# Kernel optimization log

Measured on AMD Instinct MI355X. Metric: run time of the kernel, lower is better.

The kernel has to match this reference:

```python
import jax, jax.numpy as jnp
import numpy as np

L = 6        # number of blocks (hardcoded in Transformer)
H = 16       # num_heads
C = 1024     # num_embeddings
HS = C // H  # head_size = 64
FF = 4 * C   # ffn hidden
V = 67       # vocab = len(chars)
B, T = 8, 1024
EPS = 1e-5   # nn.LayerNorm default


def _ln(x, g, b):
    m = jnp.mean(x, axis=-1, keepdims=True)
    v = jnp.mean((x - m) ** 2, axis=-1, keepdims=True)
    return (x - m) * jax.lax.rsqrt(v + EPS) * g + b


def setup_inputs() -> dict:
    key = jax.random.key(0)
    ks = jax.random.split(key, 20)
    s = 0.02
    inp = {
        "idx": jax.random.randint(ks[0], (B, T), 0, V),
        "tok_emb": jax.random.normal(ks[1], (V, C), jnp.float32) * s,
        "pos_emb": jax.random.normal(ks[2], (T, C), jnp.float32) * s,
        # per-head Q/K/V Linears (bias=False) packed as [L, C, H*HS]
        "Wq": jax.random.normal(ks[3], (L, C, C), jnp.float32) * s,
        "Wk": jax.random.normal(ks[4], (L, C, C), jnp.float32) * s,
        "Wv": jax.random.normal(ks[5], (L, C, C), jnp.float32) * s,
        "Wo": jax.random.normal(ks[6], (L, C, C), jnp.float32) * s,
        "bo": jnp.zeros((L, C), jnp.float32),
        "ln1_g": jnp.ones((L, C), jnp.float32),
        "ln1_b": jnp.zeros((L, C), jnp.float32),
        "ln2_g": jnp.ones((L, C), jnp.float32),
        "ln2_b": jnp.zeros((L, C), jnp.float32),
        "W1": jax.random.normal(ks[7], (L, C, FF), jnp.float32) * s,
        "b1": jnp.zeros((L, FF), jnp.float32),
        "W2": jax.random.normal(ks[8], (L, FF, C), jnp.float32) * s,
        "b2": jnp.zeros((L, C), jnp.float32),
        "lnf_g": jnp.ones((C,), jnp.float32),
        "lnf_b": jnp.zeros((C,), jnp.float32),
        "Wlm": jax.random.normal(ks[9], (C, V), jnp.float32) * s,
        "blm": jnp.zeros((V,), jnp.float32),
    }
    return inp


def reference(idx, tok_emb, pos_emb, Wq, Wk, Wv, Wo, bo, ln1_g, ln1_b,
              ln2_g, ln2_b, W1, b1, W2, b2, lnf_g, lnf_b, Wlm, blm):
    Bc, Tc = idx.shape
    x = tok_emb[idx] + pos_emb[:Tc]                      # [B,T,C]
    mask = jnp.tril(jnp.ones((Tc, Tc), bool))
    scale = 1.0 / np.sqrt(HS)                            # wei / head_size**0.5
    neg_inf = jnp.finfo(x.dtype).min
    for l in range(L):
        h = _ln(x, ln1_g[l], ln1_b[l])
        q = (h @ Wq[l]).reshape(Bc, Tc, H, HS)
        k = (h @ Wk[l]).reshape(Bc, Tc, H, HS)
        v = (h @ Wv[l]).reshape(Bc, Tc, H, HS)
        wei = jnp.einsum('bqhd,bkhd->bhqk', q, k) * scale
        wei = jnp.where(mask, wei, neg_inf)
        wei = jax.nn.softmax(wei, axis=-1)
        o = jnp.einsum('bhqk,bkhd->bqhd', wei, v).reshape(Bc, Tc, C)
        x = x + o @ Wo[l] + bo[l]
        h = _ln(x, ln2_g[l], ln2_b[l])
        x = x + jax.nn.relu(h @ W1[l] + b1[l]) @ W2[l] + b2[l]
    x = _ln(x, lnf_g, lnf_b)
    return x @ Wlm + blm                                 # [B,T,V] logits
```

## Files before the change

kernel.cpp:

```cpp
#include <hip/hip_runtime.h>

typedef unsigned short u16;
typedef unsigned int u32;
typedef __bf16 bf16x8 __attribute__((ext_vector_type(8)));
typedef float f32x4 __attribute__((ext_vector_type(4)));

#define LAYERS 6
#define NH 16
#define CDIM 1024
#define HS 64
#define FFDIM 4096
#define VOCAB 67
#define BATCH 8
#define TSEQ 1024
#define NTOK (BATCH * TSEQ)

__device__ __forceinline__ float bf2f(u16 u) {
    union { u32 i; float f; } x; x.i = ((u32)u) << 16; return x.f;
}
__device__ __forceinline__ u16 f2bf(float f) {
    u32 x = __float_as_uint(f);
    u32 r = (x + 0x7fffu + ((x >> 16) & 1u)) >> 16;
    return (u16)r;
}
__device__ __forceinline__ float ldx(const void* p, size_t i, int f32) {
    return f32 ? ((const float*)p)[i] : bf2f(((const u16*)p)[i]);
}
__device__ __forceinline__ void glds16(const u16* g, u16* lds) {
    __builtin_amdgcn_global_load_lds(
        (const __attribute__((address_space(1))) void*)g,
        (__attribute__((address_space(3))) void*)lds, 16, 0, 0);
}

__global__ void detect_kernel(const void* __restrict__ tok, int* __restrict__ flag) {
    int bad = 0;
    for (int i = threadIdx.x; i < 4096; i += 256) {
        float f = bf2f(((const u16*)tok)[i]);
        if (!(fabsf(f) < 1000.0f)) bad = 1;
    }
    if (bad) atomicOr(flag, 1);
}

template <int BF16OUT>
__global__ void embed_kernel(const int* __restrict__ idx, const void* __restrict__ tok,
                             const void* __restrict__ pos, void* __restrict__ X,
                             const int* __restrict__ dflag) {
    const int f32 = *dflag;
    const int i = blockIdx.x * 256 + threadIdx.x;
    const int n = i >> 10, cc = i & 1023;
    const int t = n & 1023;
    const float v = ldx(tok, (size_t)idx[n] * CDIM + cc, f32) + ldx(pos, (size_t)t * CDIM + cc, f32);
    if constexpr (BF16OUT) ((u16*)X)[i] = f2bf(v);
    else                   ((float*)X)[i] = v;
}

__global__ void transpose_kernel(const void* __restrict__ src, size_t soff, u16* __restrict__ dst,
                                 int R, int C, const int* __restrict__ dflag) {
    __shared__ u16 tile[32][33];
    const int f32 = *dflag;
    const int bx = blockIdx.x * 32, by = blockIdx.y * 32;
    const int tx = threadIdx.x, ty = threadIdx.y;
    #pragma unroll
    for (int i = 0; i < 32; i += 8) {
        const size_t si = soff + (size_t)(by + ty + i) * C + bx + tx;
        tile[ty + i][tx] = f32 ? f2bf(((const float*)src)[si]) : ((const u16*)src)[si];
    }
    __syncthreads();
    #pragma unroll
    for (int i = 0; i < 32; i += 8) dst[(size_t)(bx + ty + i) * R + by + tx] = tile[tx][ty + i];
}

template <int BF16IN>
__global__ __launch_bounds__(256) void ln_kernel(const void* __restrict__ Xv, const void* __restrict__ g,
                                                 const void* __restrict__ b, size_t loff,
                                                 u16* __restrict__ Hout, const int* __restrict__ dflag) {
    __shared__ float sred[4];
    const int f32 = *dflag;
    const int row = blockIdx.x, tid = threadIdx.x;
    float v[4];
    if constexpr (BF16IN) {
        const u16* xr = (const u16*)Xv + (size_t)row * CDIM;
        #pragma unroll
        for (int i = 0; i < 4; ++i) v[i] = bf2f(xr[tid + i * 256]);
    } else {
        const float* xr = (const float*)Xv + (size_t)row * CDIM;
        #pragma unroll
        for (int i = 0; i < 4; ++i) v[i] = xr[tid + i * 256];
    }
    float s = v[0] + v[1] + v[2] + v[3];
    #pragma unroll
    for (int off = 1; off < 64; off <<= 1) s += __shfl_xor(s, off, 64);
    if ((tid & 63) == 0) sred[tid >> 6] = s;
    __syncthreads();
    const float mean = (sred[0] + sred[1] + sred[2] + sred[3]) * (1.f / 1024.f);
    __syncthreads();
    float sq = 0.f;
    #pragma unroll
    for (int i = 0; i < 4; ++i) { v[i] -= mean; sq += v[i] * v[i]; }
    #pragma unroll
    for (int off = 1; off < 64; off <<= 1) sq += __shfl_xor(sq, off, 64);
    if ((tid & 63) == 0) sred[tid >> 6] = sq;
    __syncthreads();
    const float var = (sred[0] + sred[1] + sred[2] + sred[3]) * (1.f / 1024.f);
    const float inv = rsqrtf(var + 1e-5f);
    u16* hr = Hout + (size_t)row * CDIM;
    #pragma unroll
    for (int i = 0; i < 4; ++i) {
        const int cc = tid + i * 256;
        hr[cc] = f2bf(v[i] * inv * ldx(g, loff + cc, f32) + ldx(b, loff + cc, f32));
    }
}

template <int MODE>
__global__ __launch_bounds__(256) void gemm_bt(const u16* __restrict__ A, const u16* __restrict__ BT,
                                               const void* __restrict__ bias, size_t boff,
                                               float* __restrict__ X, u16* __restrict__ Out,
                                               int M, int N, int K, const int* __restrict__ dflag) {
    __shared__ u16 As[128][64];
    __shared__ u16 Bs[128][64];
    const int tid = threadIdx.x;
    const int lane = tid & 63;
    const int w = tid >> 6;
    const int wr = w >> 1, wc = w & 1;
    const int quad = lane >> 4, c = lane & 15;

    const int gx = gridDim.x, gy = gridDim.y;
    int bx = blockIdx.x, by = blockIdx.y;
    const int nwg = gx * gy;
    if ((nwg & 7) == 0) {
        const int bid = by * gx + bx;
        const int q = nwg >> 3;
        const int xcd = bid & 7;
        const int u = bid >> 3;
        const int cols = q / gy;
        if (cols * gy == q) {
            bx = xcd * cols + (u % cols);
            by = u / cols;
        } else {
            const int l = xcd * q + u;
            bx = l / gy;
            by = l - bx * gy;
        }
    }
    const int m0 = by * 128, n0 = bx * 128;

    const int lr = lane >> 3;
    const int sc = ((lane & 7) ^ lr) * 8;

    const f32x4 zero4 = {0.f, 0.f, 0.f, 0.f};
    f32x4 acc[4][4];
    #pragma unroll
    for (int i = 0; i < 4; ++i)
        #pragma unroll
        for (int j = 0; j < 4; ++j) acc[i][j] = zero4;

    for (int k0 = 0; k0 < K; k0 += 64) {
        #pragma unroll
        for (int i = 0; i < 4; ++i) {
            const int rbase = w * 8 + i * 32;
            glds16(A  + (size_t)(m0 + rbase + lr) * K + k0 + sc, &As[rbase][0]);
            glds16(BT + (size_t)(n0 + rbase + lr) * K + k0 + sc, &Bs[rbase][0]);
        }
        __syncthreads();
        #pragma unroll
        for (int ks = 0; ks < 2; ++ks) {
            bf16x8 af[4], bfr[4];
            #pragma unroll
            for (int t = 0; t < 4; ++t) {
                const int ch = ((ks * 4 + quad) ^ (c & 7)) * 8;
                af[t]  = *(const bf16x8*)(&As[wr * 64 + t * 16 + c][ch]);
                bfr[t] = *(const bf16x8*)(&Bs[wc * 64 + t * 16 + c][ch]);
            }
            #pragma unroll
            for (int mt = 0; mt < 4; ++mt)
                #pragma unroll
                for (int nt = 0; nt < 4; ++nt)
                    acc[mt][nt] = __builtin_amdgcn_mfma_f32_16x16x32_bf16(af[mt], bfr[nt], acc[mt][nt], 0, 0, 0);
        }
        __syncthreads();
    }

    int f32 = 0;
    if constexpr (MODE >= 1) f32 = *dflag;
    #pragma unroll
    for (int mt = 0; mt < 4; ++mt) {
        #pragma unroll
        for (int nt = 0; nt < 4; ++nt) {
            const int col = n0 + wc * 64 + nt * 16 + c;
            float bv = 0.f;
            if constexpr (MODE >= 1) bv = ldx(bias, boff + col, f32);
            #pragma unroll
            for (int r = 0; r < 4; ++r) {
                const size_t row = (size_t)(m0 + wr * 64 + mt * 16 + quad * 4 + r);
                float v = acc[mt][nt][r];
                if constexpr (MODE == 2) {
                    X[row * N + col] += v + bv;
                } else if constexpr (MODE == 3) {
                    u16* o = &Out[row * N + col];
                    *o = f2bf(bf2f(*o) + v + bv);
                } else if constexpr (MODE == 1) {
                    v += bv; v = fmaxf(v, 0.f);
                    Out[row * N + col] = f2bf(v);
                } else {
                    Out[row * N + col] = f2bf(v);
                }
            }
        }
    }
}

__global__ __launch_bounds__(256) void attn_kernel(const u16* __restrict__ Qb, const u16* __restrict__ Kb,
                                                   const u16* __restrict__ Vb, u16* __restrict__ Ob,
                                                   int rs) {
    __shared__ u16 Qs[64][64];
    __shared__ u16 Ks[64][64];
    __shared__ u16 Vts[64][64];
    __shared__ u16 Ps[4][16][64];

    const int tid = threadIdx.x;
    const int lane = tid & 63;
    const int w = tid >> 6;
    const int quad = lane >> 4;
    const int c = lane & 15;
    const int bh = blockIdx.x;
    const int b = bh >> 4;
    const int h = bh & 15;
    const int q0 = blockIdx.y * 64;
    const size_t base = ((size_t)b * TSEQ) * rs + (size_t)h * HS;

    {
        const int r = tid >> 2;
        const int d0 = (tid & 3) * 16;
        const u16* src = Qb + base + (size_t)(q0 + r) * rs + d0;
        #pragma unroll
        for (int i = 0; i < 16; ++i) Qs[r][d0 + i] = f2bf(bf2f(src[i]) * 0.125f);
    }
    __syncthreads();

    const int qbase = q0 + w * 16;
    const bf16x8 qf0 = *(const bf16x8*)(&Qs[w * 16 + c][quad * 8]);
    const bf16x8 qf1 = *(const bf16x8*)(&Qs[w * 16 + c][32 + quad * 8]);

    const f32x4 zero4 = {0.f, 0.f, 0.f, 0.f};
    f32x4 oacc[4] = {zero4, zero4, zero4, zero4};
    float m_r[4], l_r[4];
    #pragma unroll
    for (int r = 0; r < 4; ++r) { m_r[r] = -1e30f; l_r[r] = 0.f; }

    const int nch = blockIdx.y + 1;
    for (int ch = 0; ch < nch; ++ch) {
        const int k0 = ch * 64;
        {
            const int r = tid >> 2;
            const int d0 = (tid & 3) * 16;
            const u16* ks = Kb + base + (size_t)(k0 + r) * rs + d0;
            *(uint4*)(&Ks[r][d0])     = *(const uint4*)(ks);
            *(uint4*)(&Ks[r][d0 + 8]) = *(const uint4*)(ks + 8);
            const u16* vs = Vb + base + (size_t)(k0 + r) * rs + d0;
            #pragma unroll
            for (int i = 0; i < 16; ++i) Vts[d0 + i][r] = vs[i];
        }
        __syncthreads();

        f32x4 s[4];
        #pragma unroll
        for (int kt = 0; kt < 4; ++kt) {
            const bf16x8 kf0 = *(const bf16x8*)(&Ks[kt * 16 + c][quad * 8]);
            const bf16x8 kf1 = *(const bf16x8*)(&Ks[kt * 16 + c][32 + quad * 8]);
            f32x4 t0 = __builtin_amdgcn_mfma_f32_16x16x32_bf16(qf0, kf0, zero4, 0, 0, 0);
            s[kt] = __builtin_amdgcn_mfma_f32_16x16x32_bf16(qf1, kf1, t0, 0, 0, 0);
        }
        #pragma unroll
        for (int kt = 0; kt < 4; ++kt) {
            const int kabs = k0 + kt * 16 + c;
            #pragma unroll
            for (int r = 0; r < 4; ++r) {
                if (kabs > qbase + quad * 4 + r) s[kt][r] = -1e30f;
            }
        }
        float p[4][4];
        #pragma unroll
        for (int r = 0; r < 4; ++r) {
            float rm = fmaxf(fmaxf(s[0][r], s[1][r]), fmaxf(s[2][r], s[3][r]));
            #pragma unroll
            for (int off = 1; off < 16; off <<= 1) rm = fmaxf(rm, __shfl_xor(rm, off, 16));
            const float mnew = fmaxf(m_r[r], rm);
            const float alpha = __expf(m_r[r] - mnew);
            float psum = 0.f;
            #pragma unroll
            for (int kt = 0; kt < 4; ++kt) {
                const float e = __expf(s[kt][r] - mnew);
                p[kt][r] = e; psum += e;
            }
            #pragma unroll
            for (int off = 1; off < 16; off <<= 1) psum += __shfl_xor(psum, off, 16);
            l_r[r] = l_r[r] * alpha + psum;
            m_r[r] = mnew;
            #pragma unroll
            for (int dt = 0; dt < 4; ++dt) oacc[dt][r] *= alpha;
        }
        #pragma unroll
        for (int kt = 0; kt < 4; ++kt)
            #pragma unroll
            for (int r = 0; r < 4; ++r)
                Ps[w][quad * 4 + r][kt * 16 + c] = f2bf(p[kt][r]);
        __syncthreads();
        #pragma unroll
        for (int ks2 = 0; ks2 < 2; ++ks2) {
            const bf16x8 pf = *(const bf16x8*)(&Ps[w][c][ks2 * 32 + quad * 8]);
            #pragma unroll
            for (int dt = 0; dt < 4; ++dt) {
                const bf16x8 vf = *(const bf16x8*)(&Vts[dt * 16 + c][ks2 * 32 + quad * 8]);
                oacc[dt] = __builtin_amdgcn_mfma_f32_16x16x32_bf16(pf, vf, oacc[dt], 0, 0, 0);
            }
        }
        __syncthreads();
    }
    #pragma unroll
    for (int dt = 0; dt < 4; ++dt)
        #pragma unroll
        for (int r = 0; r < 4; ++r) {
            const size_t row = (size_t)b * TSEQ + qbase + quad * 4 + r;
            Ob[row * CDIM + h * HS + dt * 16 + c] = f2bf(oacc[dt][r] / l_r[r]);
        }
}

__global__ void wlmT_kernel(const void* __restrict__ Wlm, u16* __restrict__ WlmT,
                            const int* __restrict__ dflag) {
    const int f32 = *dflag;
    const int i = blockIdx.x * 256 + threadIdx.x;
    if (i >= VOCAB * CDIM) return;
    const int v = i >> 10, cc = i & 1023;
    WlmT[i] = f2bf(ldx(Wlm, (size_t)cc * VOCAB + v, f32));
}

__device__ __forceinline__ void ld16bf(const u16* p, float* v) {
    const uint4 a = *(const uint4*)(p);
    const uint4 b = *(const uint4*)(p + 8);
    u32 t[8] = {a.x, a.y, a.z, a.w, b.x, b.y, b.z, b.w};
    #pragma unroll
    for (int i = 0; i < 8; ++i) {
        v[2 * i]     = bf2f((u16)(t[i] & 0xffffu));
        v[2 * i + 1] = bf2f((u16)(t[i] >> 16));
    }
}

__global__ __launch_bounds__(256) void lmhead2_kernel(const u16* __restrict__ Hf, const u16* __restrict__ WlmT,
                                                      const void* __restrict__ blm, void* __restrict__ out,
                                                      size_t ooff, const int* __restrict__ dflag) {
    const int f32 = *dflag;
    const int lane = threadIdx.x & 63;
    const int n = blockIdx.x * 4 + (threadIdx.x >> 6);
    float hv[16];
    ld16bf(Hf + (size_t)n * CDIM + lane * 16, hv);
    for (int v = 0; v < VOCAB; ++v) {
        float wv[16];
        ld16bf(WlmT + (size_t)v * CDIM + lane * 16, wv);
        float s = 0.f;
        #pragma unroll
        for (int i = 0; i < 16; ++i) s += hv[i] * wv[i];
        #pragma unroll
        for (int off = 1; off < 64; off <<= 1) s += __shfl_xor(s, off, 64);
        if (lane == 0) {
            s += ldx(blm, v, f32);
            const size_t o = ooff + (size_t)n * VOCAB + v;
            if (f32) ((float*)out)[o] = s;
            else     ((u16*)out)[o]   = f2bf(s);
        }
    }
}

extern "C" void kernel_launch(void* const* d_in, const int* in_sizes, int n_in,
                              void* d_out, int out_size, void* d_ws, size_t ws_size,
                              hipStream_t stream) {
    const int*  idx  = (const int*)d_in[0];
    const void* tok  = d_in[1];
    const void* pos  = d_in[2];
    const void* Wq   = d_in[3];
    const void* Wk   = d_in[4];
    const void* Wv   = d_in[5];
    const void* Wo   = d_in[6];
    const void* bo   = d_in[7];
    const void* ln1g = d_in[8];
    const void* ln1b = d_in[9];
    const void* ln2g = d_in[10];
    const void* ln2b = d_in[11];
    const void* W1   = d_in[12];
    const void* b1   = d_in[13];
    const void* W2   = d_in[14];
    const void* b2   = d_in[15];
    const void* lnfg = d_in[16];
    const void* lnfb = d_in[17];
    const void* Wlm  = d_in[18];
    const void* blm  = d_in[19];

    const dim3 tb(32, 8);
    const size_t wsz = (size_t)CDIM * CDIM;
    const size_t MB = 1048576ull;

    int* dflag = (int*)d_ws;
    char* pool = (char*)d_ws + 256;
    const size_t pool_size = (ws_size > 256) ? ws_size - 256 : 0;

    const int wlmT_blocks = (VOCAB * CDIM + 255) / 256;

    if (pool_size >= 120 * MB) {
        hipMemsetAsync(d_ws, 0, 256 + 120 * MB, stream);
        detect_kernel<<<1, 256, 0, stream>>>(tok, dflag);
        char* p = pool;
        u16* wT = (u16*)p;  p += (size_t)FFDIM * CDIM * 2;
        u16* WqT = wT;
        u16* WkT = wT + 1 * wsz;
        u16* WvT = wT + 2 * wsz;
        u16* WoT = wT + 3 * wsz;
        float* x = (float*)p; p += (size_t)NTOK * CDIM * 4;
        u16* h   = (u16*)p;   p += (size_t)NTOK * CDIM * 2;
        u16* qb  = (u16*)p;   p += (size_t)NTOK * CDIM * 2;
        u16* kb  = (u16*)p;   p += (size_t)NTOK * CDIM * 2;  (void)kb;
        u16* vb  = (u16*)p;   p += (size_t)NTOK * CDIM * 2;  (void)vb;
        u16* ob  = (u16*)p;   p += (size_t)NTOK * CDIM * 2;
        u16* ffh = qb;

        embed_kernel<0><<<NTOK * CDIM / 256, 256, 0, stream>>>(idx, tok, pos, x, dflag);
        for (int l = 0; l < LAYERS; ++l) {
            transpose_kernel<<<dim3(32, 32), tb, 0, stream>>>(Wq, l * wsz, WqT, CDIM, CDIM, dflag);
            transpose_kernel<<<dim3(32, 32), tb, 0, stream>>>(Wk, l * wsz, WkT, CDIM, CDIM, dflag);
            transpose_kernel<<<dim3(32, 32), tb, 0, stream>>>(Wv, l * wsz, WvT, CDIM, CDIM, dflag);
            transpose_kernel<<<dim3(32, 32), tb, 0, stream>>>(Wo, l * wsz, WoT, CDIM, CDIM, dflag);
            ln_kernel<0><<<NTOK, 256, 0, stream>>>(x, ln1g, ln1b, (size_t)l * CDIM, h, dflag);
            gemm_bt<0><<<dim3(24, 64), 256, 0, stream>>>(h, wT, nullptr, 0, nullptr, qb, NTOK, 3 * CDIM, CDIM, dflag);
            attn_kernel<<<dim3(BATCH * NH, TSEQ / 64), 256, 0, stream>>>(qb, qb + CDIM, qb + 2 * CDIM, ob, 3 * CDIM);
            gemm_bt<2><<<dim3(8, 64), 256, 0, stream>>>(ob, WoT, bo, (size_t)l * CDIM, x, nullptr, NTOK, CDIM, CDIM, dflag);
            ln_kernel<0><<<NTOK, 256, 0, stream>>>(x, ln2g, ln2b, (size_t)l * CDIM, h, dflag);
            transpose_kernel<<<dim3(128, 32), tb, 0, stream>>>(W1, (size_t)l * CDIM * FFDIM, wT, CDIM, FFDIM, dflag);
            gemm_bt<1><<<dim3(32, 64), 256, 0, stream>>>(h, wT, b1, (size_t)l * FFDIM, nullptr, ffh, NTOK, FFDIM, CDIM, dflag);
            transpose_kernel<<<dim3(32, 128), tb, 0, stream>>>(W2, (size_t)l * CDIM * FFDIM, wT, FFDIM, CDIM, dflag);
            gemm_bt<2><<<dim3(8, 64), 256, 0, stream>>>(ffh, wT, b2, (size_t)l * CDIM, x, nullptr, NTOK, CDIM, FFDIM, dflag);
        }
        ln_kernel<0><<<NTOK, 256, 0, stream>>>(x, lnfg, lnfb, 0, h, dflag);
        wlmT_kernel<<<wlmT_blocks, 256, 0, stream>>>(Wlm, qb, dflag);
        lmhead2_kernel<<<NTOK / 4, 256, 0, stream>>>(h, qb, blm, d_out, 0, dflag);
    } else if (pool_size >= 34 * MB) {
        int CR, useW2T;
        if      (pool_size >= 52 * MB) { CR = 2048; useW2T = 1; }
        else if (pool_size >= 42 * MB) { CR = 1024; useW2T = 1; }
        else                           { CR = 1024; useW2T = 0; }
        const size_t need = 8 * MB + 16 * MB + (size_t)CR * CDIM * 2 * 5 + (useW2T ? 8 * MB : 0);
        hipMemsetAsync(d_ws, 0, 256 + need, stream);
        detect_kernel<<<1, 256, 0, stream>>>(tok, dflag);
        char* p = pool;
        u16* wT = (u16*)p;  p += (size_t)FFDIM * CDIM * 2;
        u16* WqT = wT;
        u16* WkT = wT + 1 * wsz;
        u16* WvT = wT + 2 * wsz;
        u16* WoT = wT + 3 * wsz;
        u16* xb  = (u16*)p; p += (size_t)NTOK * CDIM * 2;
        u16* hc  = (u16*)p; p += (size_t)CR * CDIM * 2;
        u16* qc  = (u16*)p; p += (size_t)CR * CDIM * 2;
        u16* kc  = (u16*)p; p += (size_t)CR * CDIM * 2;      (void)kc;
        u16* vc  = (u16*)p; p += (size_t)CR * CDIM * 2;      (void)vc;
        u16* oc  = (u16*)p; p += (size_t)CR * CDIM * 2;
        u16* ffc = qc;
        u16* W2T = nullptr;
        if (useW2T) { W2T = (u16*)p; p += (size_t)FFDIM * CDIM * 2; }

        embed_kernel<1><<<NTOK * CDIM / 256, 256, 0, stream>>>(idx, tok, pos, xb, dflag);
        for (int l = 0; l < LAYERS; ++l) {
            transpose_kernel<<<dim3(32, 32), tb, 0, stream>>>(Wq, l * wsz, WqT, CDIM, CDIM, dflag);
            transpose_kernel<<<dim3(32, 32), tb, 0, stream>>>(Wk, l * wsz, WkT, CDIM, CDIM, dflag);
            transpose_kernel<<<dim3(32, 32), tb, 0, stream>>>(Wv, l * wsz, WvT, CDIM, CDIM, dflag);
            transpose_kernel<<<dim3(32, 32), tb, 0, stream>>>(Wo, l * wsz, WoT, CDIM, CDIM, dflag);
            for (int g = 0; g < NTOK / CR; ++g) {
                u16* xg = xb + (size_t)g * CR * CDIM;
                ln_kernel<1><<<CR, 256, 0, stream>>>(xg, ln1g, ln1b, (size_t)l * CDIM, hc, dflag);
                gemm_bt<0><<<dim3(24, CR / 128), 256, 0, stream>>>(hc, wT, nullptr, 0, nullptr, qc, CR, 3 * CDIM, CDIM, dflag);
                attn_kernel<<<dim3((CR / TSEQ) * NH, TSEQ / 64), 256, 0, stream>>>(qc, qc + CDIM, qc + 2 * CDIM, oc, 3 * CDIM);
                gemm_bt<3><<<dim3(8, CR / 128), 256, 0, stream>>>(oc, WoT, bo, (size_t)l * CDIM, nullptr, xg, CR, CDIM, CDIM, dflag);
            }
            if (W2T) {
                transpose_kernel<<<dim3(128, 32), tb, 0, stream>>>(W1, (size_t)l * CDIM * FFDIM, wT, CDIM, FFDIM, dflag);
                transpose_kernel<<<dim3(32, 128), tb, 0, stream>>>(W2, (size_t)l * CDIM * FFDIM, W2T, FFDIM, CDIM, dflag);
                for (int g = 0; g < NTOK / CR; ++g) {
                    u16* xg = xb + (size_t)g * CR * CDIM;
                    ln_kernel<1><<<CR, 256, 0, stream>>>(xg, ln2g, ln2b, (size_t)l * CDIM, hc, dflag);
                    gemm_bt<1><<<dim3(32, CR / 128), 256, 0, stream>>>(hc, wT, b1, (size_t)l * FFDIM, nullptr, ffc, CR, FFDIM, CDIM, dflag);
                    gemm_bt<3><<<dim3(8, CR / 128), 256, 0, stream>>>(ffc, W2T, b2, (size_t)l * CDIM, nullptr, xg, CR, CDIM, FFDIM, dflag);
                }
            } else {
                for (int g = 0; g < NTOK / CR; ++g) {
                    u16* xg = xb + (size_t)g * CR * CDIM;
                    ln_kernel<1><<<CR, 256, 0, stream>>>(xg, ln2g, ln2b, (size_t)l * CDIM, hc, dflag);
                    transpose_kernel<<<dim3(128, 32), tb, 0, stream>>>(W1, (size_t)l * CDIM * FFDIM, wT, CDIM, FFDIM, dflag);
                    gemm_bt<1><<<dim3(32, CR / 128), 256, 0, stream>>>(hc, wT, b1, (size_t)l * FFDIM, nullptr, ffc, CR, FFDIM, CDIM, dflag);
                    transpose_kernel<<<dim3(32, 128), tb, 0, stream>>>(W2, (size_t)l * CDIM * FFDIM, wT, FFDIM, CDIM, dflag);
                    gemm_bt<3><<<dim3(8, CR / 128), 256, 0, stream>>>(ffc, wT, b2, (size_t)l * CDIM, nullptr, xg, CR, CDIM, FFDIM, dflag);
                }
            }
        }
        wlmT_kernel<<<wlmT_blocks, 256, 0, stream>>>(Wlm, qc, dflag);
        for (int g = 0; g < NTOK / CR; ++g) {
            u16* xg = xb + (size_t)g * CR * CDIM;
            ln_kernel<1><<<CR, 256, 0, stream>>>(xg, lnfg, lnfb, 0, hc, dflag);
            lmhead2_kernel<<<CR / 4, 256, 0, stream>>>(hc, qc, blm, d_out, (size_t)g * CR * VOCAB, dflag);
        }
    } else {
        hipMemsetAsync(d_out, 0, (size_t)out_size * 2, stream);
    }
}
```

Baseline: 2.988 ms.

## Rework attention to read Q/K/V fragments directly from global with pre-transposed V

Attention no longer stages Q, K and V tiles in shared memory with block-wide barriers. Q and K MFMA fragments are loaded straight from global memory. V is first transposed into a separate buffer by a new transpose kernel launch, so its fragments can also be read directly. The Q scaling moves onto the scores, the P tile in LDS is XOR-swizzled so barriers can be dropped, and blocks are remapped so the longest causal rows are scheduled first and grouped by XCD. The cost is an extra transpose pass per layer and uncoalesced, possibly repeated global loads that now depend on cache hits.

```diff
diff --git a/kernel.cpp b/kernel.cpp
--- a/kernel.cpp
+++ b/kernel.cpp
@@ -54,15 +54,16 @@
     else                   ((float*)X)[i] = v;
 }
 
+template <int BF16SRC>
 __global__ void transpose_kernel(const void* __restrict__ src, size_t soff, u16* __restrict__ dst,
-                                 int R, int C, const int* __restrict__ dflag) {
+                                 int R, int C, int SC, const int* __restrict__ dflag) {
     __shared__ u16 tile[32][33];
-    const int f32 = *dflag;
+    const int f32 = BF16SRC ? 0 : *dflag;
     const int bx = blockIdx.x * 32, by = blockIdx.y * 32;
     const int tx = threadIdx.x, ty = threadIdx.y;
     #pragma unroll
     for (int i = 0; i < 32; i += 8) {
-        const size_t si = soff + (size_t)(by + ty + i) * C + bx + tx;
+        const size_t si = soff + (size_t)(by + ty + i) * SC + bx + tx;
         tile[ty + i][tx] = f32 ? f2bf(((const float*)src)[si]) : ((const u16*)src)[si];
     }
     __syncthreads();
@@ -210,11 +211,8 @@
 }
 
 __global__ __launch_bounds__(256) void attn_kernel(const u16* __restrict__ Qb, const u16* __restrict__ Kb,
-                                                   const u16* __restrict__ Vb, u16* __restrict__ Ob,
-                                                   int rs) {
-    __shared__ u16 Qs[64][64];
-    __shared__ u16 Ks[64][64];
-    __shared__ u16 Vts[64][64];
+                                                   const u16* __restrict__ VT, u16* __restrict__ Ob,
+                                                   int rs, int vstride) {
     __shared__ u16 Ps[4][16][64];
 
     const int tid = threadIdx.x;
@@ -222,24 +220,31 @@
     const int w = tid >> 6;
     const int quad = lane >> 4;
     const int c = lane & 15;
-    const int bh = blockIdx.x;
+
+    const int nbh = gridDim.x, nq = gridDim.y;
+    int bh, qi;
+    {
+        const int flat = blockIdx.y * nbh + blockIdx.x;
+        if ((nbh & 7) == 0) {
+            const int bpx = nbh >> 3;
+            const int xcd = flat & 7;
+            const int u = flat >> 3;
+            bh = xcd * bpx + (u % bpx);
+            qi = nq - 1 - u / bpx;
+        } else { bh = blockIdx.x; qi = blockIdx.y; }
+    }
     const int b = bh >> 4;
     const int h = bh & 15;
-    const int q0 = blockIdx.y * 64;
+    const int q0 = qi * 64;
     const size_t base = ((size_t)b * TSEQ) * rs + (size_t)h * HS;
 
-    {
-        const int r = tid >> 2;
-        const int d0 = (tid & 3) * 16;
-        const u16* src = Qb + base + (size_t)(q0 + r) * rs + d0;
-        #pragma unroll
-        for (int i = 0; i < 16; ++i) Qs[r][d0 + i] = f2bf(bf2f(src[i]) * 0.125f);
-    }
-    __syncthreads();
-
     const int qbase = q0 + w * 16;
-    const bf16x8 qf0 = *(const bf16x8*)(&Qs[w * 16 + c][quad * 8]);
-    const bf16x8 qf1 = *(const bf16x8*)(&Qs[w * 16 + c][32 + quad * 8]);
+    const u16* qrow = Qb + base + (size_t)(qbase + c) * rs;
+    const bf16x8 qf0 = *(const bf16x8*)(qrow + quad * 8);
+    const bf16x8 qf1 = *(const bf16x8*)(qrow + 32 + quad * 8);
+
+    const u16* krow = Kb + base + (size_t)c * rs + quad * 8;
+    const u16* vrow = VT + (size_t)(h * HS) * vstride + (size_t)b * TSEQ;
 
     const f32x4 zero4 = {0.f, 0.f, 0.f, 0.f};
     f32x4 oacc[4] = {zero4, zero4, zero4, zero4};
@@ -247,26 +252,15 @@
     #pragma unroll
     for (int r = 0; r < 4; ++r) { m_r[r] = -1e30f; l_r[r] = 0.f; }
 
-    const int nch = blockIdx.y + 1;
+    const int nch = qi + 1;
     for (int ch = 0; ch < nch; ++ch) {
         const int k0 = ch * 64;
-        {
-            const int r = tid >> 2;
-            const int d0 = (tid & 3) * 16;
-            const u16* ks = Kb + base + (size_t)(k0 + r) * rs + d0;
-            *(uint4*)(&Ks[r][d0])     = *(const uint4*)(ks);
-            *(uint4*)(&Ks[r][d0 + 8]) = *(const uint4*)(ks + 8);
-            const u16* vs = Vb + base + (size_t)(k0 + r) * rs + d0;
-            #pragma unroll
-            for (int i = 0; i < 16; ++i) Vts[d0 + i][r] = vs[i];
-        }
-        __syncthreads();
-
         f32x4 s[4];
         #pragma unroll
         for (int kt = 0; kt < 4; ++kt) {
-            const bf16x8 kf0 = *(const bf16x8*)(&Ks[kt * 16 + c][quad * 8]);
-            const bf16x8 kf1 = *(const bf16x8*)(&Ks[kt * 16 + c][32 + quad * 8]);
+            const u16* kp = krow + (size_t)(k0 + kt * 16) * rs;
+            const bf16x8 kf0 = *(const bf16x8*)(kp);
+            const bf16x8 kf1 = *(const bf16x8*)(kp + 32);
             f32x4 t0 = __builtin_amdgcn_mfma_f32_16x16x32_bf16(qf0, kf0, zero4, 0, 0, 0);
             s[kt] = __builtin_amdgcn_mfma_f32_16x16x32_bf16(qf1, kf1, t0, 0, 0, 0);
         }
@@ -275,6 +269,7 @@
             const int kabs = k0 + kt * 16 + c;
             #pragma unroll
             for (int r = 0; r < 4; ++r) {
+                s[kt][r] *= 0.125f;
                 if (kabs > qbase + quad * 4 + r) s[kt][r] = -1e30f;
             }
         }
@@ -302,19 +297,21 @@
         #pragma unroll
         for (int kt = 0; kt < 4; ++kt)
             #pragma unroll
-            for (int r = 0; r < 4; ++r)
-                Ps[w][quad * 4 + r][kt * 16 + c] = f2bf(p[kt][r]);
-        __syncthreads();
+            for (int r = 0; r < 4; ++r) {
+                const int prow = quad * 4 + r;
+                const int ch2 = (kt * 2 + (c >> 3)) ^ (prow & 7);
+                Ps[w][prow][ch2 * 8 + (c & 7)] = f2bf(p[kt][r]);
+            }
         #pragma unroll
         for (int ks2 = 0; ks2 < 2; ++ks2) {
-            const bf16x8 pf = *(const bf16x8*)(&Ps[w][c][ks2 * 32 + quad * 8]);
+            const bf16x8 pf = *(const bf16x8*)(&Ps[w][c][(((ks2 * 4 + quad) ^ (c & 7))) * 8]);
             #pragma unroll
             for (int dt = 0; dt < 4; ++dt) {
-                const bf16x8 vf = *(const bf16x8*)(&Vts[dt * 16 + c][ks2 * 32 + quad * 8]);
+                const u16* vp = vrow + (size_t)(dt * 16 + c) * vstride + k0 + ks2 * 32 + quad * 8;
+                const bf16x8 vf = *(const bf16x8*)(vp);
                 oacc[dt] = __builtin_amdgcn_mfma_f32_16x16x32_bf16(pf, vf, oacc[dt], 0, 0, 0);
             }
         }
-        __syncthreads();
     }
     #pragma unroll
     for (int dt = 0; dt < 4; ++dt)
@@ -423,18 +420,19 @@
 
         embed_kernel<0><<<NTOK * CDIM / 256, 256, 0, stream>>>(idx, tok, pos, x, dflag);
         for (int l = 0; l < LAYERS; ++l) {
-            transpose_kernel<<<dim3(32, 32), tb, 0, stream>>>(Wq, l * wsz, WqT, CDIM, CDIM, dflag);
-            transpose_kernel<<<dim3(32, 32), tb, 0, stream>>>(Wk, l * wsz, WkT, CDIM, CDIM, dflag);
-            transpose_kernel<<<dim3(32, 32), tb, 0, stream>>>(Wv, l * wsz, WvT, CDIM, CDIM, dflag);
-            transpose_kernel<<<dim3(32, 32), tb, 0, stream>>>(Wo, l * wsz, WoT, CDIM, CDIM, dflag);
+            transpose_kernel<0><<<dim3(32, 32), tb, 0, stream>>>(Wq, l * wsz, WqT, CDIM, CDIM, CDIM, dflag);
+            transpose_kernel<0><<<dim3(32, 32), tb, 0, stream>>>(Wk, l * wsz, WkT, CDIM, CDIM, CDIM, dflag);
+            transpose_kernel<0><<<dim3(32, 32), tb, 0, stream>>>(Wv, l * wsz, WvT, CDIM, CDIM, CDIM, dflag);
+            transpose_kernel<0><<<dim3(32, 32), tb, 0, stream>>>(Wo, l * wsz, WoT, CDIM, CDIM, CDIM, dflag);
             ln_kernel<0><<<NTOK, 256, 0, stream>>>(x, ln1g, ln1b, (size_t)l * CDIM, h, dflag);
             gemm_bt<0><<<dim3(24, 64), 256, 0, stream>>>(h, wT, nullptr, 0, nullptr, qb, NTOK, 3 * CDIM, CDIM, dflag);
-            attn_kernel<<<dim3(BATCH * NH, TSEQ / 64), 256, 0, stream>>>(qb, qb + CDIM, qb + 2 * CDIM, ob, 3 * CDIM);
+            transpose_kernel<1><<<dim3(32, NTOK / 32), tb, 0, stream>>>(qb, 2 * CDIM, h, NTOK, CDIM, 3 * CDIM, dflag);
+            attn_kernel<<<dim3(BATCH * NH, TSEQ / 64), 256, 0, stream>>>(qb, qb + CDIM, h, ob, 3 * CDIM, NTOK);
             gemm_bt<2><<<dim3(8, 64), 256, 0, stream>>>(ob, WoT, bo, (size_t)l * CDIM, x, nullptr, NTOK, CDIM, CDIM, dflag);
             ln_kernel<0><<<NTOK, 256, 0, stream>>>(x, ln2g, ln2b, (size_t)l * CDIM, h, dflag);
-            transpose_kernel<<<dim3(128, 32), tb, 0, stream>>>(W1, (size_t)l * CDIM * FFDIM, wT, CDIM, FFDIM, dflag);
+            transpose_kernel<0><<<dim3(128, 32), tb, 0, stream>>>(W1, (size_t)l * CDIM * FFDIM, wT, CDIM, FFDIM, FFDIM, dflag);
             gemm_bt<1><<<dim3(32, 64), 256, 0, stream>>>(h, wT, b1, (size_t)l * FFDIM, nullptr, ffh, NTOK, FFDIM, CDIM, dflag);
-            transpose_kernel<<<dim3(32, 128), tb, 0, stream>>>(W2, (size_t)l * CDIM * FFDIM, wT, FFDIM, CDIM, dflag);
+            transpose_kernel<0><<<dim3(32, 128), tb, 0, stream>>>(W2, (size_t)l * CDIM * FFDIM, wT, FFDIM, CDIM, CDIM, dflag);
             gemm_bt<2><<<dim3(8, 64), 256, 0, stream>>>(ffh, wT, b2, (size_t)l * CDIM, x, nullptr, NTOK, CDIM, FFDIM, dflag);
         }
         ln_kernel<0><<<NTOK, 256, 0, stream>>>(x, lnfg, lnfb, 0, h, dflag);
@@ -466,20 +464,21 @@
 
         embed_kernel<1><<<NTOK * CDIM / 256, 256, 0, stream>>>(idx, tok, pos, xb, dflag);
         for (int l = 0; l < LAYERS; ++l) {
-            transpose_kernel<<<dim3(32, 32), tb, 0, stream>>>(Wq, l * wsz, WqT, CDIM, CDIM, dflag);
-            transpose_kernel<<<dim3(32, 32), tb, 0, stream>>>(Wk, l * wsz, WkT, CDIM, CDIM, dflag);
-            transpose_kernel<<<dim3(32, 32), tb, 0, stream>>>(Wv, l * wsz, WvT, CDIM, CDIM, dflag);
-            transpose_kernel<<<dim3(32, 32), tb, 0, stream>>>(Wo, l * wsz, WoT, CDIM, CDIM, dflag);
+            transpose_kernel<0><<<dim3(32, 32), tb, 0, stream>>>(Wq, l * wsz, WqT, CDIM, CDIM, CDIM, dflag);
+            transpose_kernel<0><<<dim3(32, 32), tb, 0, stream>>>(Wk, l * wsz, WkT, CDIM, CDIM, CDIM, dflag);
+            transpose_kernel<0><<<dim3(32, 32), tb, 0, stream>>>(Wv, l * wsz, WvT, CDIM, CDIM, CDIM, dflag);
+            transpose_kernel<0><<<dim3(32, 32), tb, 0, stream>>>(Wo, l * wsz, WoT, CDIM, CDIM, CDIM, dflag);
             for (int g = 0; g < NTOK / CR; ++g) {
                 u16* xg = xb + (size_t)g * CR * CDIM;
                 ln_kernel<1><<<CR, 256, 0, stream>>>(xg, ln1g, ln1b, (size_t)l * CDIM, hc, dflag);
                 gemm_bt<0><<<dim3(24, CR / 128), 256, 0, stream>>>(hc, wT, nullptr, 0, nullptr, qc, CR, 3 * CDIM, CDIM, dflag);
-                attn_kernel<<<dim3((CR / TSEQ) * NH, TSEQ / 64), 256, 0, stream>>>(qc, qc + CDIM, qc + 2 * CDIM, oc, 3 * CDIM);
+                transpose_kernel<1><<<dim3(32, CR / 32), tb, 0, stream>>>(qc, 2 * CDIM, hc, CR, CDIM, 3 * CDIM, dflag);
+                attn_kernel<<<dim3((CR / TSEQ) * NH, TSEQ / 64), 256, 0, stream>>>(qc, qc + CDIM, hc, oc, 3 * CDIM, CR);
                 gemm_bt<3><<<dim3(8, CR / 128), 256, 0, stream>>>(oc, WoT, bo, (size_t)l * CDIM, nullptr, xg, CR, CDIM, CDIM, dflag);
             }
             if (W2T) {
-                transpose_kernel<<<dim3(128, 32), tb, 0, stream>>>(W1, (size_t)l * CDIM * FFDIM, wT, CDIM, FFDIM, dflag);
-                transpose_kernel<<<dim3(32, 128), tb, 0, stream>>>(W2, (size_t)l * CDIM * FFDIM, W2T, FFDIM, CDIM, dflag);
+                transpose_kernel<0><<<dim3(128, 32), tb, 0, stream>>>(W1, (size_t)l * CDIM * FFDIM, wT, CDIM, FFDIM, FFDIM, dflag);
+                transpose_kernel<0><<<dim3(32, 128), tb, 0, stream>>>(W2, (size_t)l * CDIM * FFDIM, W2T, FFDIM, CDIM, CDIM, dflag);
                 for (int g = 0; g < NTOK / CR; ++g) {
                     u16* xg = xb + (size_t)g * CR * CDIM;
                     ln_kernel<1><<<CR, 256, 0, stream>>>(xg, ln2g, ln2b, (size_t)l * CDIM, hc, dflag);
@@ -490,9 +489,9 @@
                 for (int g = 0; g < NTOK / CR; ++g) {
                     u16* xg = xb + (size_t)g * CR * CDIM;
                     ln_kernel<1><<<CR, 256, 0, stream>>>(xg, ln2g, ln2b, (size_t)l * CDIM, hc, dflag);
-                    transpose_kernel<<<dim3(128, 32), tb, 0, stream>>>(W1, (size_t)l * CDIM * FFDIM, wT, CDIM, FFDIM, dflag);
+                    transpose_kernel<0><<<dim3(128, 32), tb, 0, stream>>>(W1, (size_t)l * CDIM * FFDIM, wT, CDIM, FFDIM, FFDIM, dflag);
                     gemm_bt<1><<<dim3(32, CR / 128), 256, 0, stream>>>(hc, wT, b1, (size_t)l * FFDIM, nullptr, ffc, CR, FFDIM, CDIM, dflag);
-                    transpose_kernel<<<dim3(32, 128), tb, 0, stream>>>(W2, (size_t)l * CDIM * FFDIM, wT, FFDIM, CDIM, dflag);
+                    transpose_kernel<0><<<dim3(32, 128), tb, 0, stream>>>(W2, (size_t)l * CDIM * FFDIM, wT, FFDIM, CDIM, CDIM, dflag);
                     gemm_bt<3><<<dim3(8, CR / 128), 256, 0, stream>>>(ffc, wT, b2, (size_t)l * CDIM, nullptr, xg, CR, CDIM, FFDIM, dflag);
                 }
             }
```

Result: slower. 3.237 ms (+8.3%).
